# Performance work log

Measured on AMD Instinct MI355X. Metric: run time of the kernel, lower is better.

The kernel has to match this reference:

```python
import jax, jax.numpy as jnp
import numpy as np

B, S, H, E = 64, 512, 1024, 10  # batch, encoder seq len, hidden, n_events
LSTM_IN = H + 1 + E  # context (H) + x (1) + sim_scores (E)


def setup_inputs() -> dict:
    key = jax.random.key(0)
    ks = jax.random.split(key, 20)
    s = 0.02
    return {
        "x": jax.random.normal(ks[0], (B, 1), jnp.float32),
        "h0": jax.random.normal(ks[1], (1, B, H), jnp.float32),
        "c0": jax.random.normal(ks[2], (1, B, H), jnp.float32),
        "encoder_output": jax.random.normal(ks[3], (B, S, H), jnp.float32),
        "W_enc": jax.random.normal(ks[4], (H, H), jnp.float32) * s,
        "W_dec": jax.random.normal(ks[5], (H, H), jnp.float32) * s,
        "w_val": jax.random.normal(ks[6], (H,), jnp.float32) * s,
        "W_gate": jax.random.normal(ks[7], (E, E), jnp.float32) * s,
        "events_mat": jax.random.normal(ks[8], (E, H), jnp.float32) * s,
        "W_ih": jax.random.normal(ks[9], (4 * H, LSTM_IN), jnp.float32) * s,
        "W_hh": jax.random.normal(ks[10], (4 * H, H), jnp.float32) * s,
        "b_ih": jax.random.normal(ks[11], (4 * H,), jnp.float32) * s,
        "b_hh": jax.random.normal(ks[12], (4 * H,), jnp.float32) * s,
        "ln_g": jnp.ones((H,), jnp.float32),
        "ln_b": jnp.zeros((H,), jnp.float32),
        "W_fin": jax.random.normal(ks[13], (1, H), jnp.float32) * s,
        "b_fin": jnp.zeros((1,), jnp.float32),
    }


def reference(x, h0, c0, encoder_output, W_enc, W_dec, w_val, W_gate,
              events_mat, W_ih, W_hh, b_ih, b_hh, ln_g, ln_b, W_fin, b_fin):
    h = h0[0]  # [B,H] (num_layers == 1)
    c = c0[0]
    # Bahdanau attention: v^T tanh(W_e enc + W_d h)
    proj = jnp.einsum('bsh,gh->bsg', encoder_output, W_enc) + (h @ W_dec.T)[:, None, :]
    attn_scores = jnp.tanh(proj) @ w_val  # [B,S]
    attn_weight = jax.nn.softmax(attn_scores, axis=1)
    context = jnp.einsum('bs,bsh->bh', attn_weight, encoder_output)  # [B,H]
    # event similarity + gate
    sim_scores = (context @ events_mat.T) @ W_gate.T  # [B,E]
    # single-step LSTM on concat(context, sim, x)
    xin = jnp.concatenate([context, sim_scores, x], axis=1)  # [B, H+E+1]
    gates = xin @ W_ih.T + b_ih + h @ W_hh.T + b_hh  # [B,4H]
    i, f, g, o = jnp.split(gates, 4, axis=1)  # torch gate order: i,f,g,o
    c_new = jax.nn.sigmoid(f) * c + jax.nn.sigmoid(i) * jnp.tanh(g)
    h_new = jax.nn.sigmoid(o) * jnp.tanh(c_new)  # [B,H]
    # LayerNorm(eps=1e-5)
    mu = jnp.mean(h_new, axis=-1, keepdims=True)
    var = jnp.mean(jnp.square(h_new - mu), axis=-1, keepdims=True)
    y = (h_new - mu) / jnp.sqrt(var + 1e-5) * ln_g + ln_b
    fin_output = y @ W_fin.T + b_fin  # [B,1]
    return fin_output, (h_new[None], c_new[None]), attn_weight, sim_scores
```

## Files before the change

### kernel.cpp

```cpp
#include <hip/hip_runtime.h>
#include <math.h>

#define Bn 64
#define Sn 512
#define Hn 1024
#define En 10
#define Mn (Bn*Sn)
#define KIN 1035
#define KP  2112

#define OUT_FIN 0
#define OUT_H   64
#define OUT_C   65600
#define OUT_AW  131136
#define OUT_SIM 163904

#define WS_ENCB  0
#define WS_WENCB 16777216
#define WS_WTS   17301504
#define WS_PART  17334272
#define WS_CTX   17596416
#define WS_WDECB 17661952
#define WS_H0B   18186240
#define WS_DPART 18219008
#define WS_WCATB 0
#define WS_GPART 4325376
#define WS_XINB  6422528

typedef __attribute__((ext_vector_type(8))) short bf16x8;
typedef __attribute__((ext_vector_type(4))) float f32x4;

#define ASYNC_CP16(gptr, lptr) \
  __builtin_amdgcn_global_load_lds((const __attribute__((address_space(1))) void*)(gptr), \
                                   (__attribute__((address_space(3))) void*)(lptr), 16, 0, 0)

static __device__ __forceinline__ unsigned short f2bf(float f) {
    union { float f; unsigned int u; } v; v.f = f;
    unsigned int r = (v.u + 0x7fffu + ((v.u >> 16) & 1u)) >> 16;
    return (unsigned short)r;
}
static __device__ __forceinline__ float bf2f(unsigned short h) {
    union { unsigned int u; float f; } v; v.u = ((unsigned int)h) << 16;
    return v.f;
}
static __device__ __forceinline__ float fast_tanh(float x) {
    float cx = fminf(15.f, fmaxf(-15.f, x));
    float e = __expf(2.f * cx);
    return (e - 1.f) * __builtin_amdgcn_rcpf(e + 1.f);
}

__global__ __launch_bounds__(256) void k_cast(const float* __restrict__ enc,
                                              const float* __restrict__ Wenc,
                                              const float* __restrict__ Wdec,
                                              const float* __restrict__ h0,
                                              unsigned short* __restrict__ encB,
                                              unsigned short* __restrict__ wencB,
                                              unsigned short* __restrict__ wdecB,
                                              unsigned short* __restrict__ h0B) {
    int bid = blockIdx.x;
    const float* src; unsigned short* dst; size_t off;
    if (bid < 16384)      { src = enc;  dst = encB;  off = (size_t)bid * 2048; }
    else if (bid < 16896) { src = Wenc; dst = wencB; off = (size_t)(bid - 16384) * 2048; }
    else if (bid < 17408) { src = Wdec; dst = wdecB; off = (size_t)(bid - 16896) * 2048; }
    else                  { src = h0;   dst = h0B;   off = (size_t)(bid - 17408) * 2048; }
    off += (size_t)threadIdx.x * 8;
    float4 v0 = *(const float4*)(src + off);
    float4 v1 = *(const float4*)(src + off + 4);
    ushort4 a; a.x = f2bf(v0.x); a.y = f2bf(v0.y); a.z = f2bf(v0.z); a.w = f2bf(v0.w);
    ushort4 b; b.x = f2bf(v1.x); b.y = f2bf(v1.y); b.z = f2bf(v1.z); b.w = f2bf(v1.w);
    *(ushort4*)(dst + off)     = a;
    *(ushort4*)(dst + off + 4) = b;
}

__global__ __launch_bounds__(256) void k1_gemm(const unsigned short* __restrict__ h0B,
                                               const unsigned short* __restrict__ wdecB,
                                               float* __restrict__ dpart) {
    __shared__ short As[4096];
    __shared__ short Bs[8192];

    const int n0 = blockIdx.x * 128;
    const int sp = blockIdx.y;
    const int kbeg = sp * 256;
    const int tid  = threadIdx.x;
    const int wave = tid >> 6;
    const int lane = tid & 63;
    const int wr = wave >> 1;
    const int wc = wave & 1;
    const int q4 = lane >> 4;
    const int ml = lane & 15;

    f32x4 acc[2][4];
#pragma unroll
    for (int i = 0; i < 2; ++i)
#pragma unroll
        for (int j = 0; j < 4; ++j) acc[i][j] = (f32x4){0.f, 0.f, 0.f, 0.f};

    const unsigned short* bTile = wdecB + (size_t)n0 * 1024;

    for (int kk = 0; kk < 4; ++kk) {
        int k0 = kbeg + kk * 64;
        __syncthreads();
#pragma unroll
        for (int t = 0; t < 2; ++t) {
            int q = wave * 2 + t;
            ASYNC_CP16(h0B + (size_t)lane * 1024 + k0 + q * 8, &As[(q * 64) * 8]);
        }
#pragma unroll
        for (int t = 0; t < 4; ++t) {
            int cb = t * 4 + wave;
            int q  = cb >> 1;
            int mb = (cb & 1) << 6;
            ASYNC_CP16(bTile + (size_t)(mb + lane) * 1024 + k0 + q * 8,
                       &Bs[(q * 128 + mb) * 8]);
        }
        __syncthreads();
#pragma unroll
        for (int s = 0; s < 2; ++s) {
            bf16x8 af[2], bfr[4];
#pragma unroll
            for (int i = 0; i < 2; ++i)
                af[i] = *(const bf16x8*)&As[((((s << 2) + q4) * 64) + wr * 32 + (i << 4) + ml) * 8];
#pragma unroll
            for (int j = 0; j < 4; ++j)
                bfr[j] = *(const bf16x8*)&Bs[((((s << 2) + q4) * 128) + wc * 64 + (j << 4) + ml) * 8];
#pragma unroll
            for (int i = 0; i < 2; ++i)
#pragma unroll
                for (int j = 0; j < 4; ++j)
                    acc[i][j] = __builtin_amdgcn_mfma_f32_16x16x32_bf16(af[i], bfr[j], acc[i][j], 0, 0, 0);
        }
    }
#pragma unroll
    for (int i = 0; i < 2; ++i)
#pragma unroll
        for (int j = 0; j < 4; ++j)
#pragma unroll
            for (int r = 0; r < 4; ++r) {
                int m = wr * 32 + (i << 4) + q4 * 4 + r;
                int n = n0 + wc * 64 + (j << 4) + ml;
                dpart[((size_t)sp * 64 + m) * 1024 + n] = acc[i][j][r];
            }
}

__global__ __launch_bounds__(512, 4) void k2_scores(const unsigned short* __restrict__ encB,
                                                    const unsigned short* __restrict__ wencB,
                                                    const float* __restrict__ dpart,
                                                    const float* __restrict__ wval,
                                                    float* __restrict__ part) {
    __shared__ short As[16384];
    __shared__ short Bs[16384];

    const int m0 = blockIdx.x * 128;
    const int n0 = blockIdx.y * 128;
    const int b  = m0 >> 9;
    const int tid  = threadIdx.x;
    const int wave = tid >> 6;
    const int lane = tid & 63;
    const int wr = wave >> 1;
    const int wc = wave & 1;
    const int q4 = lane >> 4;
    const int ml = lane & 15;

    f32x4 acc[2][4];
#pragma unroll
    for (int i = 0; i < 2; ++i)
#pragma unroll
        for (int j = 0; j < 4; ++j) acc[i][j] = (f32x4){0.f, 0.f, 0.f, 0.f};

    const unsigned short* aTile = encB  + (size_t)m0 * 1024;
    const unsigned short* bTile = wencB + (size_t)n0 * 1024;

    for (int k0 = 0; k0 < 1024; k0 += 128) {
        __syncthreads();
#pragma unroll
        for (int t = 0; t < 8; ++t) {
            int c = t * 8 + wave;
            if (c < 32) {
                int q  = c >> 1;
                int mb = (c & 1) << 6;
                ASYNC_CP16(aTile + (size_t)(mb + lane) * 1024 + k0 + q * 8,
                           &As[(q * 128 + mb) * 8]);
            } else {
                int c2 = c - 32;
                int q  = c2 >> 1;
                int mb = (c2 & 1) << 6;
                ASYNC_CP16(bTile + (size_t)(mb + lane) * 1024 + k0 + q * 8,
                           &Bs[(q * 128 + mb) * 8]);
            }
        }
        __syncthreads();
#pragma unroll
        for (int s = 0; s < 4; ++s) {
            bf16x8 af[2], bfr[4];
            int q = (s << 2) + q4;
#pragma unroll
            for (int i = 0; i < 2; ++i)
                af[i] = *(const bf16x8*)&As[((q * 128) + wr * 32 + (i << 4) + ml) * 8];
#pragma unroll
            for (int j = 0; j < 4; ++j)
                bfr[j] = *(const bf16x8*)&Bs[((q * 128) + wc * 64 + (j << 4) + ml) * 8];
#pragma unroll
            for (int i = 0; i < 2; ++i)
#pragma unroll
                for (int j = 0; j < 4; ++j)
                    acc[i][j] = __builtin_amdgcn_mfma_f32_16x16x32_bf16(af[i], bfr[j], acc[i][j], 0, 0, 0);
        }
    }

    float dpv[4], wvv[4];
#pragma unroll
    for (int j = 0; j < 4; ++j) {
        int n = n0 + wc * 64 + (j << 4) + ml;
        float d = 0.f;
#pragma unroll
        for (int sp = 0; sp < 4; ++sp) d += dpart[((size_t)sp * 64 + b) * 1024 + n];
        dpv[j] = d;
        wvv[j] = wval[n];
    }
    __syncthreads();
    float* rsum = (float*)As;
#pragma unroll
    for (int i = 0; i < 2; ++i) {
#pragma unroll
        for (int r = 0; r < 4; ++r) {
            float p = 0.f;
#pragma unroll
            for (int j = 0; j < 4; ++j) p += fast_tanh(acc[i][j][r] + dpv[j]) * wvv[j];
            p += __shfl_xor(p, 1);
            p += __shfl_xor(p, 2);
            p += __shfl_xor(p, 4);
            p += __shfl_xor(p, 8);
            if (ml == 0) rsum[wc * 128 + wr * 32 + (i << 4) + q4 * 4 + r] = p;
        }
    }
    __syncthreads();
    if (tid < 128)
        part[(size_t)blockIdx.y * Mn + m0 + tid] = rsum[tid] + rsum[128 + tid];
}

__device__ __forceinline__ float block_sum256(float v, float* red, int tid) {
#pragma unroll
    for (int off = 1; off < 64; off <<= 1) v += __shfl_xor(v, off);
    if ((tid & 63) == 0) red[tid >> 6] = v;
    __syncthreads();
    v = red[0] + red[1] + red[2] + red[3];
    __syncthreads();
    return v;
}

__global__ __launch_bounds__(256) void k3a_softmax(const float* __restrict__ part,
                                                   float* __restrict__ wts,
                                                   float* __restrict__ out) {
    int b = blockIdx.x;
    int tid = threadIdx.x;
    __shared__ float red[8];
    int s0 = tid, s1 = tid + 256;
    float v0 = 0.f, v1 = 0.f;
#pragma unroll
    for (int nb = 0; nb < 8; ++nb) {
        v0 += part[(size_t)nb * Mn + b * 512 + s0];
        v1 += part[(size_t)nb * Mn + b * 512 + s1];
    }
    float mx = fmaxf(v0, v1);
#pragma unroll
    for (int off = 1; off < 64; off <<= 1) mx = fmaxf(mx, __shfl_xor(mx, off));
    if ((tid & 63) == 0) red[tid >> 6] = mx;
    __syncthreads();
    mx = fmaxf(fmaxf(red[0], red[1]), fmaxf(red[2], red[3]));
    __syncthreads();
    float e0 = __expf(v0 - mx), e1 = __expf(v1 - mx);
    float sm = block_sum256(e0 + e1, red, tid);
    float inv = 1.0f / sm;
    float w0 = e0 * inv, w1 = e1 * inv;
    wts[b * 512 + s0] = w0;
    wts[b * 512 + s1] = w1;
    out[OUT_AW + b * 512 + s0] = w0;
    out[OUT_AW + b * 512 + s1] = w1;
}

__global__ __launch_bounds__(256) void k3b_context(const unsigned short* __restrict__ encB,
                                                   const float* __restrict__ wts,
                                                   float* __restrict__ ctxp) {
    int b  = blockIdx.y;
    int sc = blockIdx.x >> 1;
    int hh = blockIdx.x & 1;
    int h2 = (hh * 256 + threadIdx.x) * 2;
    const unsigned short* e = encB + (size_t)b * Sn * Hn + (size_t)sc * 128 * Hn + h2;
    const float* w = wts + b * 512 + sc * 128;
    float a0 = 0.f, a1 = 0.f, b0 = 0.f, b1 = 0.f;
    for (int s = 0; s < 128; s += 2) {
        unsigned int p0 = *(const unsigned int*)(e + (size_t)(s + 0) * 1024);
        unsigned int p1 = *(const unsigned int*)(e + (size_t)(s + 1) * 1024);
        a0 += w[s + 0] * bf2f((unsigned short)(p0 & 0xffffu));
        b0 += w[s + 0] * bf2f((unsigned short)(p0 >> 16));
        a1 += w[s + 1] * bf2f((unsigned short)(p1 & 0xffffu));
        b1 += w[s + 1] * bf2f((unsigned short)(p1 >> 16));
    }
    ctxp[((size_t)sc * 64 + b) * 1024 + h2]     = a0 + a1;
    ctxp[((size_t)sc * 64 + b) * 1024 + h2 + 1] = b0 + b1;
}

__global__ __launch_bounds__(256) void k3c_reduce(const float* __restrict__ ctxp,
                                                  float* __restrict__ ctx) {
    int idx = blockIdx.x * 256 + threadIdx.x;
    ctx[idx] = ctxp[idx] + ctxp[65536 + idx] + ctxp[131072 + idx] + ctxp[196608 + idx];
}

__global__ __launch_bounds__(256) void k4_sim(const float* __restrict__ ctx,
                                              const float* __restrict__ events,
                                              const float* __restrict__ Wg,
                                              float* __restrict__ out) {
    int b = blockIdx.x;
    int tid = threadIdx.x, wv = tid >> 6, lane = tid & 63;
    __shared__ float tmp[16];
    const float* c = ctx + b * 1024;
    for (int e = wv; e < 10; e += 4) {
        const float* ev = events + e * 1024;
        float a = 0.f;
#pragma unroll
        for (int kk = 0; kk < 1024; kk += 64) a += c[kk + lane] * ev[kk + lane];
#pragma unroll
        for (int off = 1; off < 64; off <<= 1) a += __shfl_xor(a, off);
        if (lane == 0) tmp[e] = a;
    }
    __syncthreads();
    if (tid < 10) {
        float s2 = 0.f;
#pragma unroll
        for (int e = 0; e < 10; ++e) s2 += Wg[tid * 10 + e] * tmp[e];
        out[OUT_SIM + b * 10 + tid] = s2;
    }
}

__global__ __launch_bounds__(256) void k_castW(const float* __restrict__ Wih,
                                               const float* __restrict__ Whh,
                                               unsigned short* __restrict__ WcatB) {
    unsigned int idx = blockIdx.x * 256 + threadIdx.x;
    unsigned int r = idx / KP;
    unsigned int k = idx - r * KP;
    float v = 0.f;
    if (k < 1035)      v = Wih[(size_t)r * 1035 + k];
    else if (k < 2059) v = Whh[(size_t)r * 1024 + (k - 1035)];
    WcatB[idx] = f2bf(v);
}

__global__ __launch_bounds__(256) void k_xinB(const float* __restrict__ ctx,
                                              const float* __restrict__ simOut,
                                              const float* __restrict__ x,
                                              const float* __restrict__ h0,
                                              unsigned short* __restrict__ xinB) {
    unsigned int idx = blockIdx.x * 256 + threadIdx.x;
    unsigned int b = idx / KP;
    unsigned int k = idx - b * KP;
    float v = 0.f;
    if (k < 1024)       v = ctx[b * 1024 + k];
    else if (k < 1034)  v = simOut[b * 10 + (k - 1024)];
    else if (k == 1034) v = x[b];
    else if (k < 2059)  v = h0[b * 1024 + (k - 1035)];
    xinB[idx] = f2bf(v);
}

__global__ __launch_bounds__(256) void k5_gemm(const unsigned short* __restrict__ xinB,
                                               const unsigned short* __restrict__ WcatB,
                                               float* __restrict__ gpart) {
    __shared__ short As[4096];
    __shared__ short Bs[8192];

    const int n0 = blockIdx.x * 128;
    const int sp = blockIdx.y;
    const int kbeg   = (sp == 0) ? 0 : (5 + (sp - 1) * 4) * 64;
    const int ksteps = (sp == 0) ? 5 : 4;
    const int tid  = threadIdx.x;
    const int wave = tid >> 6;
    const int lane = tid & 63;
    const int wr = wave >> 1;
    const int wc = wave & 1;
    const int q4 = lane >> 4;
    const int ml = lane & 15;

    f32x4 acc[2][4];
#pragma unroll
    for (int i = 0; i < 2; ++i)
#pragma unroll
        for (int j = 0; j < 4; ++j) acc[i][j] = (f32x4){0.f, 0.f, 0.f, 0.f};

    const unsigned short* bTile = WcatB + (size_t)n0 * KP;

    for (int kk = 0; kk < ksteps; ++kk) {
        int k0 = kbeg + kk * 64;
        __syncthreads();
#pragma unroll
        for (int t = 0; t < 2; ++t) {
            int q = wave * 2 + t;
            ASYNC_CP16(xinB + (size_t)lane * KP + k0 + q * 8, &As[(q * 64) * 8]);
        }
#pragma unroll
        for (int t = 0; t < 4; ++t) {
            int cb = t * 4 + wave;
            int q  = cb >> 1;
            int mb = (cb & 1) << 6;
            ASYNC_CP16(bTile + (size_t)(mb + lane) * KP + k0 + q * 8,
                       &Bs[(q * 128 + mb) * 8]);
        }
        __syncthreads();
#pragma unroll
        for (int s = 0; s < 2; ++s) {
            bf16x8 af[2], bfr[4];
#pragma unroll
            for (int i = 0; i < 2; ++i)
                af[i] = *(const bf16x8*)&As[((((s << 2) + q4) * 64) + wr * 32 + (i << 4) + ml) * 8];
#pragma unroll
            for (int j = 0; j < 4; ++j)
                bfr[j] = *(const bf16x8*)&Bs[((((s << 2) + q4) * 128) + wc * 64 + (j << 4) + ml) * 8];
#pragma unroll
            for (int i = 0; i < 2; ++i)
#pragma unroll
                for (int j = 0; j < 4; ++j)
                    acc[i][j] = __builtin_amdgcn_mfma_f32_16x16x32_bf16(af[i], bfr[j], acc[i][j], 0, 0, 0);
        }
    }
#pragma unroll
    for (int i = 0; i < 2; ++i)
#pragma unroll
        for (int j = 0; j < 4; ++j)
#pragma unroll
            for (int r = 0; r < 4; ++r) {
                int m = wr * 32 + (i << 4) + q4 * 4 + r;
                int n = n0 + wc * 64 + (j << 4) + ml;
                gpart[((size_t)sp * 64 + m) * 4096 + n] = acc[i][j][r];
            }
}

__global__ __launch_bounds__(256) void k5_fin(const float* __restrict__ gpart,
                                              const float* __restrict__ bih,
                                              const float* __restrict__ bhh,
                                              const float* __restrict__ c0,
                                              float* __restrict__ out) {
    int idx = blockIdx.x * 256 + threadIdx.x;
    int b = idx >> 10;
    int u = idx & 1023;
    float g[4];
#pragma unroll
    for (int gt = 0; gt < 4; ++gt) {
        int r = gt * 1024 + u;
        float a = bih[r] + bhh[r];
#pragma unroll
        for (int sp = 0; sp < 8; ++sp)
            a += gpart[((size_t)sp * 64 + b) * 4096 + r];
        g[gt] = a;
    }
    float cp = c0[b * 1024 + u];
    float si = 1.f / (1.f + __expf(-g[0]));
    float sf = 1.f / (1.f + __expf(-g[1]));
    float so = 1.f / (1.f + __expf(-g[3]));
    float cn = sf * cp + si * tanhf(g[2]);
    float hn = so * tanhf(cn);
    out[OUT_H + b * 1024 + u] = hn;
    out[OUT_C + b * 1024 + u] = cn;
}

__global__ __launch_bounds__(256) void k6_lnfin(const float* __restrict__ lng,
                                                const float* __restrict__ lnb,
                                                const float* __restrict__ Wfin,
                                                const float* __restrict__ bfin,
                                                float* __restrict__ out) {
    int b = blockIdx.x, tid = threadIdx.x;
    __shared__ float red[8];
    const float* h = out + OUT_H + b * 1024;
    float v0 = h[tid], v1 = h[tid + 256], v2 = h[tid + 512], v3 = h[tid + 768];
    float mu = block_sum256(v0 + v1 + v2 + v3, red, tid) * (1.f / 1024.f);
    float d0 = v0 - mu, d1 = v1 - mu, d2 = v2 - mu, d3 = v3 - mu;
    float var = block_sum256(d0 * d0 + d1 * d1 + d2 * d2 + d3 * d3, red, tid) * (1.f / 1024.f);
    float rstd = rsqrtf(var + 1e-5f);
    float acc = (d0 * rstd * lng[tid]       + lnb[tid])       * Wfin[tid]
              + (d1 * rstd * lng[tid + 256] + lnb[tid + 256]) * Wfin[tid + 256]
              + (d2 * rstd * lng[tid + 512] + lnb[tid + 512]) * Wfin[tid + 512]
              + (d3 * rstd * lng[tid + 768] + lnb[tid + 768]) * Wfin[tid + 768];
    acc = block_sum256(acc, red, tid);
    if (tid == 0) out[OUT_FIN + b] = acc + bfin[0];
}

extern "C" void kernel_launch(void* const* d_in, const int* in_sizes, int n_in,
                              void* d_out, int out_size, void* d_ws, size_t ws_size,
                              hipStream_t stream) {
    (void)in_sizes; (void)n_in; (void)out_size; (void)ws_size;
    const float* x    = (const float*)d_in[0];
    const float* h0   = (const float*)d_in[1];
    const float* c0   = (const float*)d_in[2];
    const float* enc  = (const float*)d_in[3];
    const float* Wenc = (const float*)d_in[4];
    const float* Wdec = (const float*)d_in[5];
    const float* wval = (const float*)d_in[6];
    const float* Wg   = (const float*)d_in[7];
    const float* ev   = (const float*)d_in[8];
    const float* Wih  = (const float*)d_in[9];
    const float* Whh  = (const float*)d_in[10];
    const float* bih  = (const float*)d_in[11];
    const float* bhh  = (const float*)d_in[12];
    const float* lng  = (const float*)d_in[13];
    const float* lnb  = (const float*)d_in[14];
    const float* Wfin = (const float*)d_in[15];
    const float* bfin = (const float*)d_in[16];

    float* out  = (float*)d_out;
    float* ws   = (float*)d_ws;
    unsigned short* encB  = (unsigned short*)(ws + WS_ENCB);
    unsigned short* wencB = (unsigned short*)(ws + WS_WENCB);
    unsigned short* wdecB = (unsigned short*)(ws + WS_WDECB);
    unsigned short* h0B   = (unsigned short*)(ws + WS_H0B);
    float* dpart = ws + WS_DPART;
    float* wts   = ws + WS_WTS;
    float* part  = ws + WS_PART;
    float* ctxp  = ws + WS_PART;
    float* ctx   = ws + WS_CTX;
    unsigned short* WcatB = (unsigned short*)(ws + WS_WCATB);
    float* gpart = ws + WS_GPART;
    unsigned short* xinB  = (unsigned short*)(ws + WS_XINB);

    k_cast     <<<17440, 256, 0, stream>>>(enc, Wenc, Wdec, h0, encB, wencB, wdecB, h0B);
    k1_gemm    <<<dim3(8, 4), 256, 0, stream>>>(h0B, wdecB, dpart);
    k2_scores  <<<dim3(256, 8), 512, 0, stream>>>(encB, wencB, dpart, wval, part);
    k3a_softmax<<<64, 256, 0, stream>>>(part, wts, out);
    k3b_context<<<dim3(8, 64), 256, 0, stream>>>(encB, wts, ctxp);
    k3c_reduce <<<256, 256, 0, stream>>>(ctxp, ctx);
    k4_sim     <<<64, 256, 0, stream>>>(ctx, ev, Wg, out);
    k_castW    <<<33792, 256, 0, stream>>>(Wih, Whh, WcatB);
    k_xinB     <<<528, 256, 0, stream>>>(ctx, out + OUT_SIM, x, h0, xinB);
    k5_gemm    <<<dim3(32, 8), 256, 0, stream>>>(xinB, WcatB, gpart);
    k5_fin     <<<256, 256, 0, stream>>>(gpart, bih, bhh, c0, out);
    k6_lnfin   <<<64, 256, 0, stream>>>(lng, lnb, Wfin, bfin, out);
}
```

Baseline: 466.6 us.

## Fuse small kernels, widen split-K, and reorder scores grid

Removes the context-reduce kernel and folds the 8-way context partial sum into k4_sim and k_xinB. Fuses the LSTM gate epilogue with the LayerNorm and final projection into one per-batch kernel. Doubles the split counts for the decoder GEMM and the context accumulation to expose more blocks. Flattens the scores grid so the 8 N-tiles of each M-tile are adjacent, which is meant to improve L2 reuse of encoder tiles. The trade-off is redundant partial summation in k_xinB and a fused LSTM kernel that runs on only 64 blocks.

New measurement: 462.8 us. About the same (-0.8%).

```diff
diff --git a/kernel.cpp b/kernel.cpp
--- a/kernel.cpp
+++ b/kernel.cpp
@@ -19,10 +19,10 @@
 #define WS_WENCB 16777216
 #define WS_WTS   17301504
 #define WS_PART  17334272
-#define WS_CTX   17596416
-#define WS_WDECB 17661952
-#define WS_H0B   18186240
-#define WS_DPART 18219008
+#define WS_CTXP  17334272
+#define WS_WDECB 17858560
+#define WS_H0B   18382848
+#define WS_DPART 18415616
 #define WS_WCATB 0
 #define WS_GPART 4325376
 #define WS_XINB  6422528
@@ -80,7 +80,7 @@
 
     const int n0 = blockIdx.x * 128;
     const int sp = blockIdx.y;
-    const int kbeg = sp * 256;
+    const int kbeg = sp * 128;
     const int tid  = threadIdx.x;
     const int wave = tid >> 6;
     const int lane = tid & 63;
@@ -97,7 +97,7 @@
 
     const unsigned short* bTile = wdecB + (size_t)n0 * 1024;
 
-    for (int kk = 0; kk < 4; ++kk) {
+    for (int kk = 0; kk < 2; ++kk) {
         int k0 = kbeg + kk * 64;
         __syncthreads();
 #pragma unroll
@@ -150,8 +150,10 @@
     __shared__ short As[16384];
     __shared__ short Bs[16384];
 
-    const int m0 = blockIdx.x * 128;
-    const int n0 = blockIdx.y * 128;
+    const int bid = blockIdx.x;
+    const int m0 = (bid >> 3) * 128;
+    const int nb = bid & 7;
+    const int n0 = nb * 128;
     const int b  = m0 >> 9;
     const int tid  = threadIdx.x;
     const int wave = tid >> 6;
@@ -213,7 +215,7 @@
         int n = n0 + wc * 64 + (j << 4) + ml;
         float d = 0.f;
 #pragma unroll
-        for (int sp = 0; sp < 4; ++sp) d += dpart[((size_t)sp * 64 + b) * 1024 + n];
+        for (int sp = 0; sp < 8; ++sp) d += dpart[((size_t)sp * 64 + b) * 1024 + n];
         dpv[j] = d;
         wvv[j] = wval[n];
     }
@@ -235,7 +237,7 @@
     }
     __syncthreads();
     if (tid < 128)
-        part[(size_t)blockIdx.y * Mn + m0 + tid] = rsum[tid] + rsum[128 + tid];
+        part[(size_t)nb * Mn + m0 + tid] = rsum[tid] + rsum[128 + tid];
 }
 
 __device__ __forceinline__ float block_sum256(float v, float* red, int tid) {
@@ -285,10 +287,10 @@
     int sc = blockIdx.x >> 1;
     int hh = blockIdx.x & 1;
     int h2 = (hh * 256 + threadIdx.x) * 2;
-    const unsigned short* e = encB + (size_t)b * Sn * Hn + (size_t)sc * 128 * Hn + h2;
-    const float* w = wts + b * 512 + sc * 128;
+    const unsigned short* e = encB + (size_t)b * Sn * Hn + (size_t)sc * 64 * Hn + h2;
+    const float* w = wts + b * 512 + sc * 64;
     float a0 = 0.f, a1 = 0.f, b0 = 0.f, b1 = 0.f;
-    for (int s = 0; s < 128; s += 2) {
+    for (int s = 0; s < 64; s += 2) {
         unsigned int p0 = *(const unsigned int*)(e + (size_t)(s + 0) * 1024);
         unsigned int p1 = *(const unsigned int*)(e + (size_t)(s + 1) * 1024);
         a0 += w[s + 0] * bf2f((unsigned short)(p0 & 0xffffu));
@@ -300,25 +302,28 @@
     ctxp[((size_t)sc * 64 + b) * 1024 + h2 + 1] = b0 + b1;
 }
 
-__global__ __launch_bounds__(256) void k3c_reduce(const float* __restrict__ ctxp,
-                                                  float* __restrict__ ctx) {
-    int idx = blockIdx.x * 256 + threadIdx.x;
-    ctx[idx] = ctxp[idx] + ctxp[65536 + idx] + ctxp[131072 + idx] + ctxp[196608 + idx];
-}
-
-__global__ __launch_bounds__(256) void k4_sim(const float* __restrict__ ctx,
+__global__ __launch_bounds__(256) void k4_sim(const float* __restrict__ ctxp,
                                               const float* __restrict__ events,
                                               const float* __restrict__ Wg,
                                               float* __restrict__ out) {
     int b = blockIdx.x;
     int tid = threadIdx.x, wv = tid >> 6, lane = tid & 63;
+    __shared__ float cl[1024];
     __shared__ float tmp[16];
-    const float* c = ctx + b * 1024;
+#pragma unroll
+    for (int i = 0; i < 4; ++i) {
+        int h = tid + i * 256;
+        float v = 0.f;
+#pragma unroll
+        for (int sc = 0; sc < 8; ++sc) v += ctxp[((size_t)sc * 64 + b) * 1024 + h];
+        cl[h] = v;
+    }
+    __syncthreads();
     for (int e = wv; e < 10; e += 4) {
         const float* ev = events + e * 1024;
         float a = 0.f;
 #pragma unroll
-        for (int kk = 0; kk < 1024; kk += 64) a += c[kk + lane] * ev[kk + lane];
+        for (int kk = 0; kk < 1024; kk += 64) a += cl[kk + lane] * ev[kk + lane];
 #pragma unroll
         for (int off = 1; off < 64; off <<= 1) a += __shfl_xor(a, off);
         if (lane == 0) tmp[e] = a;
@@ -344,7 +349,7 @@
     WcatB[idx] = f2bf(v);
 }
 
-__global__ __launch_bounds__(256) void k_xinB(const float* __restrict__ ctx,
+__global__ __launch_bounds__(256) void k_xinB(const float* __restrict__ ctxp,
                                               const float* __restrict__ simOut,
                                               const float* __restrict__ x,
                                               const float* __restrict__ h0,
@@ -353,7 +358,11 @@
     unsigned int b = idx / KP;
     unsigned int k = idx - b * KP;
     float v = 0.f;
-    if (k < 1024)       v = ctx[b * 1024 + k];
+    if (k < 1024) {
+        v = 0.f;
+#pragma unroll
+        for (int sc = 0; sc < 8; ++sc) v += ctxp[((size_t)sc * 64 + b) * 1024 + k];
+    }
     else if (k < 1034)  v = simOut[b * 10 + (k - 1024)];
     else if (k == 1034) v = x[b];
     else if (k < 2059)  v = h0[b * 1024 + (k - 1035)];
@@ -431,45 +440,42 @@
             }
 }
 
-__global__ __launch_bounds__(256) void k5_fin(const float* __restrict__ gpart,
-                                              const float* __restrict__ bih,
-                                              const float* __restrict__ bhh,
-                                              const float* __restrict__ c0,
-                                              float* __restrict__ out) {
-    int idx = blockIdx.x * 256 + threadIdx.x;
-    int b = idx >> 10;
-    int u = idx & 1023;
-    float g[4];
-#pragma unroll
-    for (int gt = 0; gt < 4; ++gt) {
-        int r = gt * 1024 + u;
-        float a = bih[r] + bhh[r];
-#pragma unroll
-        for (int sp = 0; sp < 8; ++sp)
-            a += gpart[((size_t)sp * 64 + b) * 4096 + r];
-        g[gt] = a;
-    }
-    float cp = c0[b * 1024 + u];
-    float si = 1.f / (1.f + __expf(-g[0]));
-    float sf = 1.f / (1.f + __expf(-g[1]));
-    float so = 1.f / (1.f + __expf(-g[3]));
-    float cn = sf * cp + si * tanhf(g[2]);
-    float hn = so * tanhf(cn);
-    out[OUT_H + b * 1024 + u] = hn;
-    out[OUT_C + b * 1024 + u] = cn;
-}
-
-__global__ __launch_bounds__(256) void k6_lnfin(const float* __restrict__ lng,
-                                                const float* __restrict__ lnb,
-                                                const float* __restrict__ Wfin,
-                                                const float* __restrict__ bfin,
-                                                float* __restrict__ out) {
+__global__ __launch_bounds__(256) void k56_lstm_ln(const float* __restrict__ gpart,
+                                                   const float* __restrict__ bih,
+                                                   const float* __restrict__ bhh,
+                                                   const float* __restrict__ c0,
+                                                   const float* __restrict__ lng,
+                                                   const float* __restrict__ lnb,
+                                                   const float* __restrict__ Wfin,
+                                                   const float* __restrict__ bfin,
+                                                   float* __restrict__ out) {
     int b = blockIdx.x, tid = threadIdx.x;
     __shared__ float red[8];
-    const float* h = out + OUT_H + b * 1024;
-    float v0 = h[tid], v1 = h[tid + 256], v2 = h[tid + 512], v3 = h[tid + 768];
-    float mu = block_sum256(v0 + v1 + v2 + v3, red, tid) * (1.f / 1024.f);
-    float d0 = v0 - mu, d1 = v1 - mu, d2 = v2 - mu, d3 = v3 - mu;
+    float hn[4];
+#pragma unroll
+    for (int r = 0; r < 4; ++r) {
+        int u = tid + (r << 8);
+        float g[4];
+#pragma unroll
+        for (int gt = 0; gt < 4; ++gt) {
+            int rr = gt * 1024 + u;
+            float a = bih[rr] + bhh[rr];
+#pragma unroll
+            for (int sp = 0; sp < 8; ++sp)
+                a += gpart[((size_t)sp * 64 + b) * 4096 + rr];
+            g[gt] = a;
+        }
+        float cp = c0[b * 1024 + u];
+        float si = 1.f / (1.f + __expf(-g[0]));
+        float sf = 1.f / (1.f + __expf(-g[1]));
+        float so = 1.f / (1.f + __expf(-g[3]));
+        float cn = sf * cp + si * tanhf(g[2]);
+        hn[r] = so * tanhf(cn);
+        out[OUT_H + b * 1024 + u] = hn[r];
+        out[OUT_C + b * 1024 + u] = cn;
+    }
+    float mu = block_sum256(hn[0] + hn[1] + hn[2] + hn[3], red, tid) * (1.f / 1024.f);
+    float d0 = hn[0] - mu, d1 = hn[1] - mu, d2 = hn[2] - mu, d3 = hn[3] - mu;
     float var = block_sum256(d0 * d0 + d1 * d1 + d2 * d2 + d3 * d3, red, tid) * (1.f / 1024.f);
     float rstd = rsqrtf(var + 1e-5f);
     float acc = (d0 * rstd * lng[tid]       + lnb[tid])       * Wfin[tid]
@@ -511,22 +517,19 @@
     float* dpart = ws + WS_DPART;
     float* wts   = ws + WS_WTS;
     float* part  = ws + WS_PART;
-    float* ctxp  = ws + WS_PART;
-    float* ctx   = ws + WS_CTX;
+    float* ctxp  = ws + WS_CTXP;
     unsigned short* WcatB = (unsigned short*)(ws + WS_WCATB);
     float* gpart = ws + WS_GPART;
     unsigned short* xinB  = (unsigned short*)(ws + WS_XINB);
 
     k_cast     <<<17440, 256, 0, stream>>>(enc, Wenc, Wdec, h0, encB, wencB, wdecB, h0B);
-    k1_gemm    <<<dim3(8, 4), 256, 0, stream>>>(h0B, wdecB, dpart);
-    k2_scores  <<<dim3(256, 8), 512, 0, stream>>>(encB, wencB, dpart, wval, part);
+    k1_gemm    <<<dim3(8, 8), 256, 0, stream>>>(h0B, wdecB, dpart);
+    k2_scores  <<<2048, 512, 0, stream>>>(encB, wencB, dpart, wval, part);
     k3a_softmax<<<64, 256, 0, stream>>>(part, wts, out);
-    k3b_context<<<dim3(8, 64), 256, 0, stream>>>(encB, wts, ctxp);
-    k3c_reduce <<<256, 256, 0, stream>>>(ctxp, ctx);
-    k4_sim     <<<64, 256, 0, stream>>>(ctx, ev, Wg, out);
+    k3b_context<<<dim3(16, 64), 256, 0, stream>>>(encB, wts, ctxp);
+    k4_sim     <<<64, 256, 0, stream>>>(ctxp, ev, Wg, out);
     k_castW    <<<33792, 256, 0, stream>>>(Wih, Whh, WcatB);
-    k_xinB     <<<528, 256, 0, stream>>>(ctx, out + OUT_SIM, x, h0, xinB);
+    k_xinB     <<<528, 256, 0, stream>>>(ctxp, out + OUT_SIM, x, h0, xinB);
     k5_gemm    <<<dim3(32, 8), 256, 0, stream>>>(xinB, WcatB, gpart);
-    k5_fin     <<<256, 256, 0, stream>>>(gpart, bih, bhh, c0, out);
-    k6_lnfin   <<<64, 256, 0, stream>>>(lng, lnb, Wfin, bfin, out);
-}
+    k56_lstm_ln<<<64, 256, 0, stream>>>(gpart, bih, bhh, c0, lng, lnb, Wfin, bfin, out);
+}
```
